# Performance work log

Measured on AMD Instinct MI355X. Metric: run time of the kernel, lower is better.

The kernel has to match this reference:

```python
import jax, jax.numpy as jnp
import numpy as np

MARGIN = 1.0
EPS = 1e-8  # torch.cosine_similarity default eps


def _cosine(a, b):
    num = jnp.sum(a * b, axis=1)
    den = jnp.maximum(jnp.linalg.norm(a, axis=1) * jnp.linalg.norm(b, axis=1), EPS)
    return num / den


def setup_inputs() -> dict:
    key = jax.random.key(0)
    k1, k2 = jax.random.split(key)
    B, D = 8192, 512
    anchor = jax.random.normal(k1, (B, D), dtype=jnp.float32)
    positive = jax.random.normal(k2, (B, D), dtype=jnp.float32)
    return {"anchor": anchor, "positive": positive}


def reference(anchor, positive):
    B = positive.shape[0]
    a_n = anchor / jnp.linalg.norm(anchor, axis=1, keepdims=True)
    p_n = positive / jnp.linalg.norm(positive, axis=1, keepdims=True)
    sim = a_n @ p_n.T                      # [B, B] cosine similarity
    mask = 1.0 - jnp.eye(B, dtype=sim.dtype)
    sim = sim * mask                       # zero diagonal
    # margin branch of NegariveSampler (margin=1): abs(sim - margin), zeros -> -inf, argmax
    score = jnp.abs(sim - MARGIN) * mask
    score = jnp.where(score == 0.0, -jnp.inf, score)
    neg_idx = jnp.argmax(score, axis=1)    # [B]
    neg = p_n[neg_idx]                     # gather normalized positives as negatives
    cos_ap = _cosine(anchor, positive)
    cos_an = _cosine(anchor, neg)
    loss = jax.nn.relu(MARGIN + cos_ap - cos_an)
    return loss.mean()
```

## Files before the change

kernel.cpp:

```cpp
#include <hip/hip_runtime.h>
#include <stdint.h>

typedef int   i32x8 __attribute__((ext_vector_type(8)));
typedef float f32x4 __attribute__((ext_vector_type(4)));

#define B_ROWS 8192
#define D_DIM  512

__device__ __forceinline__ uint32_t enc_f32(float f) {
  uint32_t s = __float_as_uint(f);
  return (s & 0x80000000u) ? ~s : (s | 0x80000000u);
}
__device__ __forceinline__ float dec_f32(uint32_t e) {
  uint32_t s = (e & 0x80000000u) ? (e ^ 0x80000000u) : ~e;
  return __uint_as_float(s);
}

__global__ __launch_bounds__(256) void norm_kernel(
    const float* __restrict__ anchor, const float* __restrict__ positive,
    uint32_t* __restrict__ a8, uint32_t* __restrict__ p8,
    float* __restrict__ cos_ap, uint32_t* __restrict__ minenc)
{
  const int wave = threadIdx.x >> 6, lane = threadIdx.x & 63;
  const int r = blockIdx.x * 4 + wave;

  const float4* av = (const float4*)(anchor   + (size_t)r * D_DIM) + lane * 2;
  const float4* pv = (const float4*)(positive + (size_t)r * D_DIM) + lane * 2;
  float4 a0 = av[0], a1 = av[1];
  float4 p0 = pv[0], p1 = pv[1];

  float sa = a0.x*a0.x + a0.y*a0.y + a0.z*a0.z + a0.w*a0.w
           + a1.x*a1.x + a1.y*a1.y + a1.z*a1.z + a1.w*a1.w;
  float sp = p0.x*p0.x + p0.y*p0.y + p0.z*p0.z + p0.w*p0.w
           + p1.x*p1.x + p1.y*p1.y + p1.z*p1.z + p1.w*p1.w;
  float dp = a0.x*p0.x + a0.y*p0.y + a0.z*p0.z + a0.w*p0.w
           + a1.x*p1.x + a1.y*p1.y + a1.z*p1.z + a1.w*p1.w;

#pragma unroll
  for (int d = 1; d < 64; d <<= 1) {
    sa += __shfl_xor(sa, d);
    sp += __shfl_xor(sp, d);
    dp += __shfl_xor(dp, d);
  }

  const float na = sqrtf(sa), np = sqrtf(sp);
  const float ia = 1.0f / na, ip = 1.0f / np;

  float na0 = a0.x*ia, na1 = a0.y*ia, na2 = a0.z*ia, na3 = a0.w*ia;
  float na4 = a1.x*ia, na5 = a1.y*ia, na6 = a1.z*ia, na7 = a1.w*ia;
  float np0 = p0.x*ip, np1 = p0.y*ip, np2 = p0.z*ip, np3 = p0.w*ip;
  float np4 = p1.x*ip, np5 = p1.y*ip, np6 = p1.z*ip, np7 = p1.w*ip;

  uint32_t aw0 = __builtin_amdgcn_cvt_pk_fp8_f32(na0, na1, 0,  false);
  aw0          = __builtin_amdgcn_cvt_pk_fp8_f32(na2, na3, aw0, true);
  uint32_t aw1 = __builtin_amdgcn_cvt_pk_fp8_f32(na4, na5, 0,  false);
  aw1          = __builtin_amdgcn_cvt_pk_fp8_f32(na6, na7, aw1, true);
  uint32_t pw0 = __builtin_amdgcn_cvt_pk_fp8_f32(np0, np1, 0,  false);
  pw0          = __builtin_amdgcn_cvt_pk_fp8_f32(np2, np3, pw0, true);
  uint32_t pw1 = __builtin_amdgcn_cvt_pk_fp8_f32(np4, np5, 0,  false);
  pw1          = __builtin_amdgcn_cvt_pk_fp8_f32(np6, np7, pw1, true);

  ((uint2*)a8)[(size_t)r * 64 + lane] = make_uint2(aw0, aw1);
  ((uint2*)p8)[(size_t)r * 64 + lane] = make_uint2(pw0, pw1);

  if (lane == 0) {
    cos_ap[r] = dp / fmaxf(na * np, 1e-8f);
    minenc[r] = 0xFFFFFFFFu;
  }
}

__device__ __forceinline__ void load16_to_lds(const void* g, void* l) {
  __builtin_amdgcn_global_load_lds(
      (__attribute__((address_space(1))) uint32_t*)(uintptr_t)(g),
      (__attribute__((address_space(3))) uint32_t*)(uintptr_t)(l),
      16, 0, 0);
}

__global__ __launch_bounds__(256, 2) void simmin_kernel(
    const uint8_t* __restrict__ a8, const uint8_t* __restrict__ p8,
    uint32_t* __restrict__ minenc)
{
  __shared__ __attribute__((aligned(16))) uint8_t Alds[2][128 * 128];
  __shared__ __attribute__((aligned(16))) uint8_t Plds[2][128 * 128];
  __shared__ float redmin[256];

  const int tid  = threadIdx.x;
  const int lane = tid & 63;
  const int wave = tid >> 6;
  const int waveM = wave >> 1, waveN = wave & 1;
  const int quad = lane >> 4;
  const int l15  = lane & 15;

  const int bid = blockIdx.x;
  const int blockRow = (bid & 7) * 8 + ((bid >> 3) & 7);
  const int blockCol = bid >> 6;

  f32x4 acc[4][4];
  const f32x4 zero = {0.f, 0.f, 0.f, 0.f};
#pragma unroll
  for (int i = 0; i < 4; i++)
#pragma unroll
    for (int j = 0; j < 4; j++) acc[i][j] = zero;

  const int srow = lane >> 3;
  const int sk   = (lane & 7) ^ srow;
  const uint8_t* aBase = a8 + (size_t)(blockRow * 128) * D_DIM;
  const uint8_t* pBase = p8 + (size_t)(blockCol * 128) * D_DIM;

  auto stage = [&](int k0, int buf) {
#pragma unroll
    for (int c = 0; c < 4; c++) {
      const int chunk = wave * 4 + c;
      const size_t goff = (size_t)(chunk * 8 + srow) * D_DIM + k0 + sk * 16;
      load16_to_lds(aBase + goff, &Alds[buf][chunk * 1024]);
      load16_to_lds(pBase + goff, &Plds[buf][chunk * 1024]);
    }
  };

  stage(0, 0);

#pragma unroll
  for (int k = 0; k < 4; k++) {
    __syncthreads();
    const int buf = k & 1;

    i32x8 af[4], bfr[4];
#pragma unroll
    for (int mf = 0; mf < 4; mf++) {
      const int r = waveM * 64 + mf * 16 + l15;
      const int rx = r & 7;
      const int4 lo = *(const int4*)&Alds[buf][r * 128 + (((quad * 2 + 0) ^ rx) * 16)];
      const int4 hi = *(const int4*)&Alds[buf][r * 128 + (((quad * 2 + 1) ^ rx) * 16)];
      af[mf] = (i32x8){lo.x, lo.y, lo.z, lo.w, hi.x, hi.y, hi.z, hi.w};
    }
#pragma unroll
    for (int nf = 0; nf < 4; nf++) {
      const int r = waveN * 64 + nf * 16 + l15;
      const int rx = r & 7;
      const int4 lo = *(const int4*)&Plds[buf][r * 128 + (((quad * 2 + 0) ^ rx) * 16)];
      const int4 hi = *(const int4*)&Plds[buf][r * 128 + (((quad * 2 + 1) ^ rx) * 16)];
      bfr[nf] = (i32x8){lo.x, lo.y, lo.z, lo.w, hi.x, hi.y, hi.z, hi.w};
    }

    if (k < 3) stage((k + 1) * 128, (k + 1) & 1);

#pragma unroll
    for (int mf = 0; mf < 4; mf++)
#pragma unroll
      for (int nf = 0; nf < 4; nf++)
        acc[mf][nf] = __builtin_amdgcn_mfma_scale_f32_16x16x128_f8f6f4(
            af[mf], bfr[nf], acc[mf][nf],
            0, 0,
            0, 0x7F7F7F7F,
            0, 0x7F7F7F7F);
  }

  const int rowTileBase = blockRow * 128 + waveM * 64;
  const int colTileBase = blockCol * 128 + waveN * 64;

  float rm[4][4];
#pragma unroll
  for (int mf = 0; mf < 4; mf++)
#pragma unroll
    for (int r = 0; r < 4; r++) rm[mf][r] = 3.0e38f;

#pragma unroll
  for (int mf = 0; mf < 4; mf++) {
#pragma unroll
    for (int nf = 0; nf < 4; nf++) {
      const int col = colTileBase + nf * 16 + l15;
#pragma unroll
      for (int r = 0; r < 4; r++) {
        const int row = rowTileBase + mf * 16 + quad * 4 + r;
        const float v = acc[mf][nf][r];
        rm[mf][r] = (row == col) ? rm[mf][r] : fminf(rm[mf][r], v);
      }
    }
  }
#pragma unroll
  for (int d = 1; d < 16; d <<= 1)
#pragma unroll
    for (int mf = 0; mf < 4; mf++)
#pragma unroll
      for (int r = 0; r < 4; r++)
        rm[mf][r] = fminf(rm[mf][r], __shfl_xor(rm[mf][r], d));

  if (l15 == 0) {
#pragma unroll
    for (int mf = 0; mf < 4; mf++)
#pragma unroll
      for (int r = 0; r < 4; r++)
        redmin[waveN * 128 + waveM * 64 + mf * 16 + quad * 4 + r] = rm[mf][r];
  }
  __syncthreads();

  if (tid < 128) {
    const float m = fminf(redmin[tid], redmin[128 + tid]);
    atomicMin(&minenc[blockRow * 128 + tid], enc_f32(m));
  }
}

__global__ __launch_bounds__(1024) void finalize_kernel(
    const uint32_t* __restrict__ minenc, const float* __restrict__ cos_ap,
    float* __restrict__ out)
{
  float sum = 0.0f;
#pragma unroll
  for (int r = threadIdx.x; r < B_ROWS; r += 1024)
    sum += fmaxf(0.0f, 1.0f + cos_ap[r] - dec_f32(minenc[r]));

#pragma unroll
  for (int d = 1; d < 64; d <<= 1) sum += __shfl_xor(sum, d);
  __shared__ float s[16];
  if ((threadIdx.x & 63) == 0) s[threadIdx.x >> 6] = sum;
  __syncthreads();
  if (threadIdx.x < 64) {
    float t = (threadIdx.x < 16) ? s[threadIdx.x] : 0.0f;
#pragma unroll
    for (int d = 1; d < 16; d <<= 1) t += __shfl_xor(t, d);
    if (threadIdx.x == 0) out[0] = t * (1.0f / (float)B_ROWS);
  }
}

extern "C" void kernel_launch(void* const* d_in, const int* in_sizes, int n_in,
                              void* d_out, int out_size, void* d_ws, size_t ws_size,
                              hipStream_t stream) {
  const float* anchor   = (const float*)d_in[0];
  const float* positive = (const float*)d_in[1];

  char* ws = (char*)d_ws;
  uint32_t* a8     = (uint32_t*)(ws);
  uint32_t* p8     = (uint32_t*)(ws + (4ull << 20));
  float*    cos_ap = (float*)(ws + (8ull << 20));
  uint32_t* minenc = (uint32_t*)(ws + (8ull << 20) + (32ull << 10));
  float*    out = (float*)d_out;

  norm_kernel<<<B_ROWS / 4, 256, 0, stream>>>(anchor, positive, a8, p8,
                                              cos_ap, minenc);
  simmin_kernel<<<4096, 256, 0, stream>>>((const uint8_t*)a8,
                                          (const uint8_t*)p8, minenc);
  finalize_kernel<<<1, 1024, 0, stream>>>(minenc, cos_ap, out);
}
```

Before: 125.1 us.

## Enlarge similarity-min GEMM tile to 256x256 with 8 waves per block

```diff
diff --git a/kernel.cpp b/kernel.cpp
--- a/kernel.cpp
+++ b/kernel.cpp
@@ -6,6 +6,10 @@
 
 #define B_ROWS 8192
 #define D_DIM  512
+#define BM 256
+#define BN 256
+#define BK 128
+#define N_BLOCKS 1024
 
 __device__ __forceinline__ uint32_t enc_f32(float f) {
   uint32_t s = __float_as_uint(f);
@@ -76,36 +80,37 @@
       16, 0, 0);
 }
 
-__global__ __launch_bounds__(256, 2) void simmin_kernel(
+__global__ __launch_bounds__(512, 2) void simmin_kernel(
     const uint8_t* __restrict__ a8, const uint8_t* __restrict__ p8,
     uint32_t* __restrict__ minenc)
 {
-  __shared__ __attribute__((aligned(16))) uint8_t Alds[2][128 * 128];
-  __shared__ __attribute__((aligned(16))) uint8_t Plds[2][128 * 128];
-  __shared__ float redmin[256];
+  __shared__ __attribute__((aligned(16))) uint8_t Alds[2][BM * BK];
+  __shared__ __attribute__((aligned(16))) uint8_t Plds[2][BN * BK];
+  __shared__ float redmin[2][4][128];
 
   const int tid  = threadIdx.x;
   const int lane = tid & 63;
   const int wave = tid >> 6;
-  const int waveM = wave >> 1, waveN = wave & 1;
+  const int waveM = wave >> 2;
+  const int waveN = wave & 3;
   const int quad = lane >> 4;
   const int l15  = lane & 15;
 
   const int bid = blockIdx.x;
-  const int blockRow = (bid & 7) * 8 + ((bid >> 3) & 7);
-  const int blockCol = bid >> 6;
-
-  f32x4 acc[4][4];
+  const int blockRow = (bid & 7) * 4 + ((bid >> 3) & 3);
+  const int blockCol = bid >> 5;
+
+  f32x4 acc[8][4];
   const f32x4 zero = {0.f, 0.f, 0.f, 0.f};
 #pragma unroll
-  for (int i = 0; i < 4; i++)
+  for (int i = 0; i < 8; i++)
 #pragma unroll
     for (int j = 0; j < 4; j++) acc[i][j] = zero;
 
   const int srow = lane >> 3;
   const int sk   = (lane & 7) ^ srow;
-  const uint8_t* aBase = a8 + (size_t)(blockRow * 128) * D_DIM;
-  const uint8_t* pBase = p8 + (size_t)(blockCol * 128) * D_DIM;
+  const uint8_t* aBase = a8 + (size_t)(blockRow * BM) * D_DIM;
+  const uint8_t* pBase = p8 + (size_t)(blockCol * BN) * D_DIM;
 
   auto stage = [&](int k0, int buf) {
 #pragma unroll
@@ -121,51 +126,49 @@
 
 #pragma unroll
   for (int k = 0; k < 4; k++) {
+    const int buf = k & 1;
     __syncthreads();
-    const int buf = k & 1;
-
-    i32x8 af[4], bfr[4];
-#pragma unroll
-    for (int mf = 0; mf < 4; mf++) {
-      const int r = waveM * 64 + mf * 16 + l15;
-      const int rx = r & 7;
-      const int4 lo = *(const int4*)&Alds[buf][r * 128 + (((quad * 2 + 0) ^ rx) * 16)];
-      const int4 hi = *(const int4*)&Alds[buf][r * 128 + (((quad * 2 + 1) ^ rx) * 16)];
-      af[mf] = (i32x8){lo.x, lo.y, lo.z, lo.w, hi.x, hi.y, hi.z, hi.w};
-    }
+
+    i32x8 bfr[4];
 #pragma unroll
     for (int nf = 0; nf < 4; nf++) {
       const int r = waveN * 64 + nf * 16 + l15;
       const int rx = r & 7;
-      const int4 lo = *(const int4*)&Plds[buf][r * 128 + (((quad * 2 + 0) ^ rx) * 16)];
-      const int4 hi = *(const int4*)&Plds[buf][r * 128 + (((quad * 2 + 1) ^ rx) * 16)];
+      const int4 lo = *(const int4*)&Plds[buf][r * BK + (((quad * 2 + 0) ^ rx) * 16)];
+      const int4 hi = *(const int4*)&Plds[buf][r * BK + (((quad * 2 + 1) ^ rx) * 16)];
       bfr[nf] = (i32x8){lo.x, lo.y, lo.z, lo.w, hi.x, hi.y, hi.z, hi.w};
     }
 
-    if (k < 3) stage((k + 1) * 128, (k + 1) & 1);
-
-#pragma unroll
-    for (int mf = 0; mf < 4; mf++)
+    if (k < 3) stage((k + 1) * BK, buf ^ 1);
+
+#pragma unroll
+    for (int mf = 0; mf < 8; mf++) {
+      const int r = waveM * 128 + mf * 16 + l15;
+      const int rx = r & 7;
+      const int4 lo = *(const int4*)&Alds[buf][r * BK + (((quad * 2 + 0) ^ rx) * 16)];
+      const int4 hi = *(const int4*)&Alds[buf][r * BK + (((quad * 2 + 1) ^ rx) * 16)];
+      const i32x8 af = (i32x8){lo.x, lo.y, lo.z, lo.w, hi.x, hi.y, hi.z, hi.w};
 #pragma unroll
       for (int nf = 0; nf < 4; nf++)
         acc[mf][nf] = __builtin_amdgcn_mfma_scale_f32_16x16x128_f8f6f4(
-            af[mf], bfr[nf], acc[mf][nf],
+            af, bfr[nf], acc[mf][nf],
             0, 0,
             0, 0x7F7F7F7F,
             0, 0x7F7F7F7F);
-  }
-
-  const int rowTileBase = blockRow * 128 + waveM * 64;
-  const int colTileBase = blockCol * 128 + waveN * 64;
-
-  float rm[4][4];
-#pragma unroll
-  for (int mf = 0; mf < 4; mf++)
+    }
+  }
+
+  const int rowTileBase = blockRow * BM + waveM * 128;
+  const int colTileBase = blockCol * BN + waveN * 64;
+
+  float rm[8][4];
+#pragma unroll
+  for (int mf = 0; mf < 8; mf++)
 #pragma unroll
     for (int r = 0; r < 4; r++) rm[mf][r] = 3.0e38f;
 
 #pragma unroll
-  for (int mf = 0; mf < 4; mf++) {
+  for (int mf = 0; mf < 8; mf++) {
 #pragma unroll
     for (int nf = 0; nf < 4; nf++) {
       const int col = colTileBase + nf * 16 + l15;
@@ -180,23 +183,25 @@
 #pragma unroll
   for (int d = 1; d < 16; d <<= 1)
 #pragma unroll
-    for (int mf = 0; mf < 4; mf++)
+    for (int mf = 0; mf < 8; mf++)
 #pragma unroll
       for (int r = 0; r < 4; r++)
         rm[mf][r] = fminf(rm[mf][r], __shfl_xor(rm[mf][r], d));
 
   if (l15 == 0) {
 #pragma unroll
-    for (int mf = 0; mf < 4; mf++)
+    for (int mf = 0; mf < 8; mf++)
 #pragma unroll
       for (int r = 0; r < 4; r++)
-        redmin[waveN * 128 + waveM * 64 + mf * 16 + quad * 4 + r] = rm[mf][r];
+        redmin[waveM][waveN][mf * 16 + quad * 4 + r] = rm[mf][r];
   }
   __syncthreads();
 
-  if (tid < 128) {
-    const float m = fminf(redmin[tid], redmin[128 + tid]);
-    atomicMin(&minenc[blockRow * 128 + tid], enc_f32(m));
+  if (tid < 256) {
+    const int wm = tid >> 7, idx = tid & 127;
+    const float m = fminf(fminf(redmin[wm][0][idx], redmin[wm][1][idx]),
+                          fminf(redmin[wm][2][idx], redmin[wm][3][idx]));
+    atomicMin(&minenc[blockRow * BM + tid], enc_f32(m));
   }
 }
 
@@ -237,7 +242,7 @@
 
   norm_kernel<<<B_ROWS / 4, 256, 0, stream>>>(anchor, positive, a8, p8,
                                               cos_ap, minenc);
-  simmin_kernel<<<4096, 256, 0, stream>>>((const uint8_t*)a8,
-                                          (const uint8_t*)p8, minenc);
+  simmin_kernel<<<N_BLOCKS, 512, 0, stream>>>((const uint8_t*)a8,
+                                              (const uint8_t*)p8, minenc);
   finalize_kernel<<<1, 1024, 0, stream>>>(minenc, cos_ap, out);
 }
```

After: 125.9 us. No clear change (+0.6%).
